# Performance work log

Hardware: AMD Instinct MI355X
Metric: run time of the kernel (lower is better)

Reference implementation:

```python
import jax, jax.numpy as jnp
import numpy as np

N_NODES = 50000
N_EDGES = 800000
D = 64
EPS = 1e-12  # torch F.normalize eps


def edge_softmax(e, dst, n):
    # softmax over incoming edges of each dst node, per feature channel
    m = jax.ops.segment_max(e, dst, num_segments=n)          # [N, D]
    ex = jnp.exp(e - m[dst])                                 # [E, D]
    s = jax.ops.segment_sum(ex, dst, num_segments=n)         # [N, D]
    return ex / s[dst]


def gat_layer(h, src, dst, W_src, b_src, W_dst, b_dst, n):
    # attention logits: u_mul_v
    e = h[src] * h[dst]                                      # [E, D]
    alpha = edge_softmax(e, dst, n)                          # [E, D]
    # transformed features (fc_dst computed in source but unused downstream)
    feat_src = jax.nn.relu(h @ W_src.T + b_src)              # [N, D]
    _feat_dst = jax.nn.relu(h @ W_dst.T + b_dst)             # [N, D] (dead, kept for fidelity)
    # message: u_mul_e, then scatter-sum to dst
    msg = feat_src[src] * alpha                              # [E, D]
    return jax.ops.segment_sum(msg, dst, num_segments=n)     # [N, D]


def l2_normalize(x):
    nrm = jnp.sqrt(jnp.sum(x * x, axis=1, keepdims=True))
    return x / jnp.maximum(nrm, EPS)


def setup_inputs() -> dict:
    key = jax.random.key(0)
    ks = jax.random.split(key, 10)
    scale = 1.0 / np.sqrt(D)
    return {
        "node_ids": jax.random.randint(ks[0], (N_NODES,), 0, N_NODES),
        "src": jax.random.randint(ks[1], (N_EDGES,), 0, N_NODES),
        "dst": jax.random.randint(ks[2], (N_EDGES,), 0, N_NODES),
        "embed_table": jax.random.normal(ks[3], (N_NODES, D), jnp.float32) * 0.1,
        "W_src_0": jax.random.normal(ks[4], (D, D), jnp.float32) * scale,
        "b_src_0": jnp.zeros((D,), jnp.float32),
        "W_dst_0": jax.random.normal(ks[5], (D, D), jnp.float32) * scale,
        "b_dst_0": jnp.zeros((D,), jnp.float32),
        "W_src_1": jax.random.normal(ks[6], (D, D), jnp.float32) * scale,
        "b_src_1": jnp.zeros((D,), jnp.float32),
        "W_dst_1": jax.random.normal(ks[7], (D, D), jnp.float32) * scale,
        "b_dst_1": jnp.zeros((D,), jnp.float32),
    }


def reference(node_ids, src, dst, embed_table,
              W_src_0, b_src_0, W_dst_0, b_dst_0,
              W_src_1, b_src_1, W_dst_1, b_dst_1):
    n = node_ids.shape[0]
    h0 = embed_table[node_ids]                               # [N, D]
    h1 = gat_layer(h0, src, dst, W_src_0, b_src_0, W_dst_0, b_dst_0, n)
    h2 = gat_layer(h1, src, dst, W_src_1, b_src_1, W_dst_1, b_dst_1, n)
    # cache = [h0, norm(h1), norm(h2)]; h passed forward unnormalized
    return jnp.concatenate([h0, l2_normalize(h1), l2_normalize(h2)], axis=1)  # [N, 3D]
```

## Files before the change

kernel.cpp:

```cpp
#include <hip/hip_runtime.h>
#include <math.h>

#define NN 50000
#define NE 800000
#define DD 64
#define FC_BLOCKS 782
#define N4 12500
#define ZB 49

typedef __attribute__((ext_vector_type(8))) short short8v;
typedef __attribute__((ext_vector_type(4))) float floatx4;

__device__ __forceinline__ unsigned bf16r(float x) {
  unsigned u = __float_as_uint(x);
  return (u + 0x7fffu + ((u >> 16) & 1u)) >> 16;
}


__global__ void k_hist(const int4* __restrict__ dst4, int* __restrict__ deg,
                       int4* __restrict__ pos4) {
  int q = blockIdx.x * 256 + threadIdx.x;
  if (q >= NE / 4) return;
  int4 dn = dst4[q];
  int4 p;
  p.x = atomicAdd(&deg[dn.x], 1);
  p.y = atomicAdd(&deg[dn.y], 1);
  p.z = atomicAdd(&deg[dn.z], 1);
  p.w = atomicAdd(&deg[dn.w], 1);
  pos4[q] = p;
}

__global__ void k_scan1(const int* __restrict__ deg, int* __restrict__ rp,
                        int* __restrict__ bsum) {
  __shared__ int woff[16];
  int t = threadIdx.x;
  int i = blockIdx.x * 1024 + t;
  int v = (i < NN) ? deg[i] : 0;
  int lane = t & 63, w = t >> 6;
  int sc = v;
#pragma unroll
  for (int off = 1; off < 64; off <<= 1) {
    int x = __shfl_up(sc, off, 64);
    if (lane >= off) sc += x;
  }
  if (lane == 63) woff[w] = sc;
  __syncthreads();
  if (t < 16) {
    int ws = woff[t];
    int s2 = ws;
#pragma unroll
    for (int off = 1; off < 16; off <<= 1) {
      int x = __shfl_up(s2, off, 64);
      if (t >= off) s2 += x;
    }
    woff[t] = s2 - ws;
    if (t == 15) bsum[blockIdx.x] = s2;
  }
  __syncthreads();
  if (i < NN) rp[i] = sc - v + woff[w];
}

__global__ void k_scan3(int* __restrict__ rp, const int* __restrict__ bsum) {
  __shared__ int soff;
  if (threadIdx.x < 64) {
    int v = ((int)threadIdx.x < (int)blockIdx.x) ? bsum[threadIdx.x] : 0;
#pragma unroll
    for (int off = 32; off > 0; off >>= 1) v += __shfl_xor(v, off, 64);
    if (threadIdx.x == 0) soff = v;
  }
  __syncthreads();
  int i = blockIdx.x * 1024 + threadIdx.x;
  if (i < NN) rp[i] += soff;
  if (i == 0) rp[NN] = NE;
}

__global__ void k_scatter(const int4* __restrict__ src4, const int4* __restrict__ dst4,
                          const int* __restrict__ rp, const int4* __restrict__ pos4,
                          int* __restrict__ ssrc) {
  int q = blockIdx.x * 256 + threadIdx.x;
  if (q >= NE / 4) return;
  int4 s = src4[q], dn = dst4[q], p = pos4[q];
  ssrc[rp[dn.x] + p.x] = s.x;
  ssrc[rp[dn.y] + p.y] = s.y;
  ssrc[rp[dn.z] + p.z] = s.z;
  ssrc[rp[dn.w] + p.w] = s.w;
}

__global__ void __launch_bounds__(256) k_fc_mfma(const float* __restrict__ h,
                                                 const int* __restrict__ ids,
                                                 const float* __restrict__ W,
                                                 const float* __restrict__ b,
                                                 unsigned* __restrict__ hfb,
                                                 int4* __restrict__ zbuf, int n4) {
  if (blockIdx.x >= FC_BLOCKS) {
    int i = (blockIdx.x - FC_BLOCKS) * 256 + threadIdx.x;
    if (i < n4) zbuf[i] = make_int4(0, 0, 0, 0);
    return;
  }
  int lane = threadIdx.x & 63;
  int wid = threadIdx.x >> 6;
  int nbase = blockIdx.x * 64 + wid * 16;
  if (nbase >= NN) return;
  int r16 = lane & 15, kg = lane >> 4;

  int rowA = ids ? ids[nbase + r16] : (nbase + r16);
  const float* hrow = h + (size_t)rowA * DD;
  short8v afr[2];
#pragma unroll
  for (int kt = 0; kt < 2; ++kt) {
    int k0 = kt * 32 + kg * 8;
#pragma unroll
    for (int i = 0; i < 8; ++i) afr[kt][i] = (short)bf16r(hrow[k0 + i]);
  }
  int orow[4];
#pragma unroll
  for (int r = 0; r < 4; ++r) {
    int node = nbase + kg * 4 + r;
    orow[r] = ids ? ids[node] : node;
  }
  short8v bfr[4][2];
#pragma unroll
  for (int dt = 0; dt < 4; ++dt) {
    const float* wrow = W + (dt * 16 + r16) * 64;
#pragma unroll
    for (int kt = 0; kt < 2; ++kt) {
      int k0 = kt * 32 + kg * 8;
#pragma unroll
      for (int i = 0; i < 8; ++i) bfr[dt][kt][i] = (short)bf16r(wrow[k0 + i]);
    }
  }
#pragma unroll
  for (int dt = 0; dt < 4; ++dt) {
    floatx4 acc = {0.f, 0.f, 0.f, 0.f};
    acc = __builtin_amdgcn_mfma_f32_16x16x32_bf16(afr[0], bfr[dt][0], acc, 0, 0, 0);
    acc = __builtin_amdgcn_mfma_f32_16x16x32_bf16(afr[1], bfr[dt][1], acc, 0, 0, 0);
    int d = dt * 16 + r16;
    float bias = b[d];
#pragma unroll
    for (int r = 0; r < 4; ++r) {
      int node = nbase + kg * 4 + r;
      float feat = fmaxf(acc[r] + bias, 0.f);
      float hv = h[(size_t)orow[r] * DD + d];
      hfb[node * DD + d] = bf16r(hv) | (bf16r(feat) << 16);
    }
  }
}

template <bool FINAL>
__global__ void __launch_bounds__(256)
k_edge_t(const unsigned* __restrict__ hfb, const float* __restrict__ h,
         const int* __restrict__ ids, const int* __restrict__ rp,
         const int* __restrict__ ssrc, float* __restrict__ outp, int ostride,
         const float* __restrict__ emb, const int* __restrict__ fids,
         const float* __restrict__ h1) {
  int d = threadIdx.x & 63;
  int node = __builtin_amdgcn_readfirstlane(blockIdx.x * 4 + (threadIdx.x >> 6));
  int beg = __builtin_amdgcn_readfirstlane(rp[node]);
  int end = __builtin_amdgcn_readfirstlane(rp[node + 1]);
  int hrow = ids ? __builtin_amdgcn_readfirstlane(ids[node]) : node;
  float hd = h[(size_t)hrow * DD + d] * 1.44269504f;
  const unsigned* hfb_d = hfb + d;
  float s[8] = {0.f, 0.f, 0.f, 0.f, 0.f, 0.f, 0.f, 0.f};
  float a[8] = {0.f, 0.f, 0.f, 0.f, 0.f, 0.f, 0.f, 0.f};
  int lim = end - 1;
  for (int p = beg; p < end; p += 8) {
    unsigned v[8];
#pragma unroll
    for (int j = 0; j < 8; ++j) {
      int q = p + j;
      q = (q > lim) ? lim : q;
      int sq = __builtin_amdgcn_readfirstlane(ssrc[q]);
      v[j] = hfb_d[(size_t)sq * DD];
    }
#pragma unroll
    for (int j = 0; j < 8; ++j) {
      float hv = __uint_as_float(v[j] << 16);
      float fv = __uint_as_float(v[j] & 0xffff0000u);
      float ex = __builtin_amdgcn_exp2f(hv * hd);
      s[j] += ex;
      a[j] = fmaf(fv, ex, a[j]);
    }
  }
  float ss = ((s[0] + s[1]) + (s[2] + s[3])) + ((s[4] + s[5]) + (s[6] + s[7]));
  float aa = ((a[0] + a[1]) + (a[2] + a[3])) + ((a[4] + a[5]) + (a[6] + a[7]));
  int deg = end - beg;
  if (deg > 0) {
    int dups = (8 - (deg & 7)) & 7;
    if (dups) {
      unsigned vL = hfb_d[(size_t)__builtin_amdgcn_readfirstlane(ssrc[lim]) * DD];
      float hvL = __uint_as_float(vL << 16);
      float fvL = __uint_as_float(vL & 0xffff0000u);
      float exL = __builtin_amdgcn_exp2f(hvL * hd);
      float fd = (float)dups;
      ss = fmaf(-fd, exL, ss);
      aa = fmaf(-fd * fvL, exL, aa);
    }
  }
  float hval = (deg > 0) ? aa / ss : 0.f;
  if (!FINAL) {
    outp[(size_t)node * ostride + d] = hval;
  } else {
    float v1 = h1[(size_t)node * DD + d];
    float s1 = v1 * v1, s2 = hval * hval;
#pragma unroll
    for (int off = 32; off > 0; off >>= 1) {
      s1 += __shfl_xor(s1, off, 64);
      s2 += __shfl_xor(s2, off, 64);
    }
    outp[node * 192 + d] = emb[(size_t)fids[node] * DD + d];
    outp[node * 192 + 64 + d] = v1 / fmaxf(sqrtf(s1), 1e-12f);
    outp[node * 192 + 128 + d] = hval / fmaxf(sqrtf(s2), 1e-12f);
  }
}


extern "C" void kernel_launch(void* const* d_in, const int* in_sizes, int n_in,
                              void* d_out, int out_size, void* d_ws, size_t ws_size,
                              hipStream_t stream) {
  const int* node_ids = (const int*)d_in[0];
  const int* src = (const int*)d_in[1];
  const int* dst = (const int*)d_in[2];
  const float* emb = (const float*)d_in[3];
  const float* W0 = (const float*)d_in[4];
  const float* b0 = (const float*)d_in[5];
  const float* W1 = (const float*)d_in[8];
  const float* b1 = (const float*)d_in[9];
  float* out = (float*)d_out;

  size_t o = 0;
  auto alloc = [&](size_t nbytes) {
    char* p = (char*)d_ws + o;
    o += (nbytes + 255) & ~(size_t)255;
    return (void*)p;
  };
  float* h1 = (float*)alloc((size_t)NN * DD * 4);
  unsigned* hfb = (unsigned*)alloc((size_t)NN * DD * 4);
  int* deg = (int*)alloc((size_t)(NN + 12) * 4);
  int* rp = (int*)alloc((size_t)(NN + 1) * 4);
  int* bsum = (int*)alloc(64 * 4);
  int* ssrc = (int*)alloc((size_t)NE * 4);
  int* pos = (int*)alloc((size_t)NE * 4);
  (void)o; (void)ws_size; (void)in_sizes; (void)n_in; (void)out_size;

  k_fc_mfma<<<FC_BLOCKS + ZB, 256, 0, stream>>>(emb, node_ids, W0, b0, hfb,
                                                (int4*)deg, N4);
  k_hist<<<(NE / 4 + 255) / 256, 256, 0, stream>>>((const int4*)dst, deg, (int4*)pos);
  int NB = (NN + 1023) / 1024;
  k_scan1<<<NB, 1024, 0, stream>>>(deg, rp, bsum);
  k_scan3<<<NB, 1024, 0, stream>>>(rp, bsum);
  k_scatter<<<(NE / 4 + 255) / 256, 256, 0, stream>>>(
      (const int4*)src, (const int4*)dst, rp, (const int4*)pos, ssrc);

  k_edge_t<false><<<(NN + 3) / 4, 256, 0, stream>>>(
      hfb, emb, node_ids, rp, ssrc, h1, DD, nullptr, nullptr, nullptr);
  k_fc_mfma<<<FC_BLOCKS, 256, 0, stream>>>(h1, nullptr, W1, b1, hfb, nullptr, 0);
  k_edge_t<true><<<(NN + 3) / 4, 256, 0, stream>>>(
      hfb, h1, nullptr, rp, ssrc, out, 0, emb, node_ids, h1);
}
```

Measured before the change: 161.8 us.

## Merge scan kernels and process two edges per wave in edge aggregation

Replaces the two-pass prefix scan with a single kernel in which each block redundantly sums all preceding degrees, removing one launch and the block-sum buffer. The degree buffer is enlarged and zeroed past NN so that rp[NN] comes out of the scan directly. The edge kernel now has each half-wave handle a different edge, with every lane covering two channels through 8-byte loads. The loop therefore takes 16 edges per iteration and combines the two halves with a cross-half shuffle at the end. This is meant to double the edges in flight per wave and halve the loop trip count, at the cost of more padding waste for low-degree nodes and more complex duplicate correction.

```diff
diff --git a/kernel.cpp b/kernel.cpp
--- a/kernel.cpp
+++ b/kernel.cpp
@@ -5,7 +5,7 @@
 #define NE 800000
 #define DD 64
 #define FC_BLOCKS 782
-#define N4 12500
+#define N4 12503
 #define ZB 49
 
 typedef __attribute__((ext_vector_type(8))) short short8v;
@@ -30,13 +30,27 @@
   pos4[q] = p;
 }
 
-__global__ void k_scan1(const int* __restrict__ deg, int* __restrict__ rp,
-                        int* __restrict__ bsum) {
+__global__ void k_scan(const int* __restrict__ deg, int* __restrict__ rp) {
+  __shared__ int wred[16];
   __shared__ int woff[16];
+  __shared__ int sbase;
   int t = threadIdx.x;
-  int i = blockIdx.x * 1024 + t;
+  int lane = t & 63, w = t >> 6;
+  int blockStart = blockIdx.x << 10;
+  int acc = 0;
+  for (int i = t; i < blockStart; i += 1024) acc += deg[i];
+#pragma unroll
+  for (int off = 32; off > 0; off >>= 1) acc += __shfl_xor(acc, off, 64);
+  if (lane == 0) wred[w] = acc;
+  __syncthreads();
+  if (t == 0) {
+    int b = 0;
+#pragma unroll
+    for (int k = 0; k < 16; ++k) b += wred[k];
+    sbase = b;
+  }
+  int i = blockStart + t;
   int v = (i < NN) ? deg[i] : 0;
-  int lane = t & 63, w = t >> 6;
   int sc = v;
 #pragma unroll
   for (int off = 1; off < 64; off <<= 1) {
@@ -54,24 +68,9 @@
       if (t >= off) s2 += x;
     }
     woff[t] = s2 - ws;
-    if (t == 15) bsum[blockIdx.x] = s2;
   }
   __syncthreads();
-  if (i < NN) rp[i] = sc - v + woff[w];
-}
-
-__global__ void k_scan3(int* __restrict__ rp, const int* __restrict__ bsum) {
-  __shared__ int soff;
-  if (threadIdx.x < 64) {
-    int v = ((int)threadIdx.x < (int)blockIdx.x) ? bsum[threadIdx.x] : 0;
-#pragma unroll
-    for (int off = 32; off > 0; off >>= 1) v += __shfl_xor(v, off, 64);
-    if (threadIdx.x == 0) soff = v;
-  }
-  __syncthreads();
-  int i = blockIdx.x * 1024 + threadIdx.x;
-  if (i < NN) rp[i] += soff;
-  if (i == 0) rp[NN] = NE;
+  if (i <= NN) rp[i] = sc - v + woff[w] + sbase;
 }
 
 __global__ void k_scatter(const int4* __restrict__ src4, const int4* __restrict__ dst4,
@@ -153,63 +152,100 @@
          const int* __restrict__ ssrc, float* __restrict__ outp, int ostride,
          const float* __restrict__ emb, const int* __restrict__ fids,
          const float* __restrict__ h1) {
-  int d = threadIdx.x & 63;
+  int lane = threadIdx.x & 63;
+  int half = lane >> 5;
+  int c = lane & 31;
   int node = __builtin_amdgcn_readfirstlane(blockIdx.x * 4 + (threadIdx.x >> 6));
   int beg = __builtin_amdgcn_readfirstlane(rp[node]);
   int end = __builtin_amdgcn_readfirstlane(rp[node + 1]);
   int hrow = ids ? __builtin_amdgcn_readfirstlane(ids[node]) : node;
-  float hd = h[(size_t)hrow * DD + d] * 1.44269504f;
-  const unsigned* hfb_d = hfb + d;
-  float s[8] = {0.f, 0.f, 0.f, 0.f, 0.f, 0.f, 0.f, 0.f};
-  float a[8] = {0.f, 0.f, 0.f, 0.f, 0.f, 0.f, 0.f, 0.f};
+  float2 hdv = *(const float2*)(h + (size_t)hrow * DD + 2 * c);
+  float hd0 = hdv.x * 1.44269504f;
+  float hd1 = hdv.y * 1.44269504f;
   int lim = end - 1;
-  for (int p = beg; p < end; p += 8) {
-    unsigned v[8];
+  float sA[8] = {0.f, 0.f, 0.f, 0.f, 0.f, 0.f, 0.f, 0.f};
+  float aA[8] = {0.f, 0.f, 0.f, 0.f, 0.f, 0.f, 0.f, 0.f};
+  float sB[8] = {0.f, 0.f, 0.f, 0.f, 0.f, 0.f, 0.f, 0.f};
+  float aB[8] = {0.f, 0.f, 0.f, 0.f, 0.f, 0.f, 0.f, 0.f};
+  for (int p = beg; p < end; p += 16) {
+    uint2 v[8];
 #pragma unroll
     for (int j = 0; j < 8; ++j) {
-      int q = p + j;
-      q = (q > lim) ? lim : q;
-      int sq = __builtin_amdgcn_readfirstlane(ssrc[q]);
-      v[j] = hfb_d[(size_t)sq * DD];
+      int q0 = p + 2 * j;
+      q0 = (q0 > lim) ? lim : q0;
+      int q1 = p + 2 * j + 1;
+      q1 = (q1 > lim) ? lim : q1;
+      int s0 = __builtin_amdgcn_readfirstlane(ssrc[q0]);
+      int s1 = __builtin_amdgcn_readfirstlane(ssrc[q1]);
+      int sq = half ? s1 : s0;
+      v[j] = *(const uint2*)(hfb + (size_t)sq * DD + 2 * c);
     }
 #pragma unroll
     for (int j = 0; j < 8; ++j) {
-      float hv = __uint_as_float(v[j] << 16);
-      float fv = __uint_as_float(v[j] & 0xffff0000u);
-      float ex = __builtin_amdgcn_exp2f(hv * hd);
-      s[j] += ex;
-      a[j] = fmaf(fv, ex, a[j]);
-    }
-  }
-  float ss = ((s[0] + s[1]) + (s[2] + s[3])) + ((s[4] + s[5]) + (s[6] + s[7]));
-  float aa = ((a[0] + a[1]) + (a[2] + a[3])) + ((a[4] + a[5]) + (a[6] + a[7]));
+      float hv0 = __uint_as_float(v[j].x << 16);
+      float fv0 = __uint_as_float(v[j].x & 0xffff0000u);
+      float hv1 = __uint_as_float(v[j].y << 16);
+      float fv1 = __uint_as_float(v[j].y & 0xffff0000u);
+      float e0 = __builtin_amdgcn_exp2f(hv0 * hd0);
+      float e1 = __builtin_amdgcn_exp2f(hv1 * hd1);
+      sA[j] += e0;
+      aA[j] = fmaf(fv0, e0, aA[j]);
+      sB[j] += e1;
+      aB[j] = fmaf(fv1, e1, aB[j]);
+    }
+  }
+  float ss0 = ((sA[0] + sA[1]) + (sA[2] + sA[3])) + ((sA[4] + sA[5]) + (sA[6] + sA[7]));
+  float aa0 = ((aA[0] + aA[1]) + (aA[2] + aA[3])) + ((aA[4] + aA[5]) + (aA[6] + aA[7]));
+  float ss1 = ((sB[0] + sB[1]) + (sB[2] + sB[3])) + ((sB[4] + sB[5]) + (sB[6] + sB[7]));
+  float aa1 = ((aB[0] + aB[1]) + (aB[2] + aB[3])) + ((aB[4] + aB[5]) + (aB[6] + aB[7]));
   int deg = end - beg;
   if (deg > 0) {
-    int dups = (8 - (deg & 7)) & 7;
-    if (dups) {
-      unsigned vL = hfb_d[(size_t)__builtin_amdgcn_readfirstlane(ssrc[lim]) * DD];
-      float hvL = __uint_as_float(vL << 16);
-      float fvL = __uint_as_float(vL & 0xffff0000u);
-      float exL = __builtin_amdgcn_exp2f(hvL * hd);
-      float fd = (float)dups;
-      ss = fmaf(-fd, exL, ss);
-      aa = fmaf(-fd * fvL, exL, aa);
-    }
-  }
-  float hval = (deg > 0) ? aa / ss : 0.f;
+    int rem = deg & 15;
+    if (rem) {
+      int dups0 = (rem & 1) ? (16 - rem) >> 1 : (17 - rem) >> 1;
+      int dups1 = (16 - rem) - dups0;
+      float fd = (float)(half ? dups1 : dups0);
+      int sL = __builtin_amdgcn_readfirstlane(ssrc[lim]);
+      uint2 vL = *(const uint2*)(hfb + (size_t)sL * DD + 2 * c);
+      float hvL0 = __uint_as_float(vL.x << 16);
+      float fvL0 = __uint_as_float(vL.x & 0xffff0000u);
+      float hvL1 = __uint_as_float(vL.y << 16);
+      float fvL1 = __uint_as_float(vL.y & 0xffff0000u);
+      float eL0 = __builtin_amdgcn_exp2f(hvL0 * hd0);
+      float eL1 = __builtin_amdgcn_exp2f(hvL1 * hd1);
+      ss0 = fmaf(-fd, eL0, ss0);
+      aa0 = fmaf(-fd * fvL0, eL0, aa0);
+      ss1 = fmaf(-fd, eL1, ss1);
+      aa1 = fmaf(-fd * fvL1, eL1, aa1);
+    }
+    ss0 += __shfl_xor(ss0, 32, 64);
+    aa0 += __shfl_xor(aa0, 32, 64);
+    ss1 += __shfl_xor(ss1, 32, 64);
+    aa1 += __shfl_xor(aa1, 32, 64);
+  }
+  float hv0 = (deg > 0) ? aa0 / ss0 : 0.f;
+  float hv1 = (deg > 0) ? aa1 / ss1 : 0.f;
   if (!FINAL) {
-    outp[(size_t)node * ostride + d] = hval;
+    if (half == 0)
+      *(float2*)(outp + (size_t)node * ostride + 2 * c) = make_float2(hv0, hv1);
   } else {
-    float v1 = h1[(size_t)node * DD + d];
-    float s1 = v1 * v1, s2 = hval * hval;
-#pragma unroll
-    for (int off = 32; off > 0; off >>= 1) {
-      s1 += __shfl_xor(s1, off, 64);
-      s2 += __shfl_xor(s2, off, 64);
-    }
-    outp[node * 192 + d] = emb[(size_t)fids[node] * DD + d];
-    outp[node * 192 + 64 + d] = v1 / fmaxf(sqrtf(s1), 1e-12f);
-    outp[node * 192 + 128 + d] = hval / fmaxf(sqrtf(s2), 1e-12f);
+    float2 v1 = *(const float2*)(h1 + (size_t)node * DD + 2 * c);
+    float ps1 = v1.x * v1.x + v1.y * v1.y;
+    float ps2 = hv0 * hv0 + hv1 * hv1;
+#pragma unroll
+    for (int off = 16; off > 0; off >>= 1) {
+      ps1 += __shfl_xor(ps1, off, 64);
+      ps2 += __shfl_xor(ps2, off, 64);
+    }
+    float inv1 = 1.f / fmaxf(sqrtf(ps1), 1e-12f);
+    float inv2 = 1.f / fmaxf(sqrtf(ps2), 1e-12f);
+    if (half == 0) {
+      int fr = __builtin_amdgcn_readfirstlane(fids[node]);
+      float2 e2 = *(const float2*)(emb + (size_t)fr * DD + 2 * c);
+      *(float2*)(outp + node * 192 + 2 * c) = e2;
+      *(float2*)(outp + node * 192 + 64 + 2 * c) = make_float2(v1.x * inv1, v1.y * inv1);
+      *(float2*)(outp + node * 192 + 128 + 2 * c) = make_float2(hv0 * inv2, hv1 * inv2);
+    }
   }
 }
 
@@ -235,9 +271,8 @@
   };
   float* h1 = (float*)alloc((size_t)NN * DD * 4);
   unsigned* hfb = (unsigned*)alloc((size_t)NN * DD * 4);
-  int* deg = (int*)alloc((size_t)(NN + 12) * 4);
+  int* deg = (int*)alloc((size_t)N4 * 16);
   int* rp = (int*)alloc((size_t)(NN + 1) * 4);
-  int* bsum = (int*)alloc(64 * 4);
   int* ssrc = (int*)alloc((size_t)NE * 4);
   int* pos = (int*)alloc((size_t)NE * 4);
   (void)o; (void)ws_size; (void)in_sizes; (void)n_in; (void)out_size;
@@ -246,8 +281,7 @@
                                                 (int4*)deg, N4);
   k_hist<<<(NE / 4 + 255) / 256, 256, 0, stream>>>((const int4*)dst, deg, (int4*)pos);
   int NB = (NN + 1023) / 1024;
-  k_scan1<<<NB, 1024, 0, stream>>>(deg, rp, bsum);
-  k_scan3<<<NB, 1024, 0, stream>>>(rp, bsum);
+  k_scan<<<NB, 1024, 0, stream>>>(deg, rp);
   k_scatter<<<(NE / 4 + 255) / 256, 256, 0, stream>>>(
       (const int4*)src, (const int4*)dst, rp, (const int4*)pos, ssrc);
 
```

Result: slower. 169.3 us (+4.7%).

## Fuse scan into single kernel and software-pipeline edge gather loads

Applied to the files above, without the earlier changes.

Merges the two-pass exclusive scan into one kernel in which each block first reduces all preceding degrees itself, removing a launch and the block-sum buffer. rp[NN] is now written by the scan, so the deg buffer is padded and the zeroing count raised to keep index NN zero. The edge aggregation loop is double-buffered: the next eight gathered rows are loaded while the current ones go through exp and accumulate. The padding correction reuses the last computed exp instead of reloading it. Later scan blocks repeat redundant prefix reads, and the doubled load registers may lower occupancy.

```diff
diff --git a/kernel.cpp b/kernel.cpp
--- a/kernel.cpp
+++ b/kernel.cpp
@@ -5,7 +5,7 @@
 #define NE 800000
 #define DD 64
 #define FC_BLOCKS 782
-#define N4 12500
+#define N4 12503
 #define ZB 49
 
 typedef __attribute__((ext_vector_type(8))) short short8v;
@@ -30,13 +30,27 @@
   pos4[q] = p;
 }
 
-__global__ void k_scan1(const int* __restrict__ deg, int* __restrict__ rp,
-                        int* __restrict__ bsum) {
+__global__ void k_scan(const int* __restrict__ deg, int* __restrict__ rp) {
+  __shared__ int wred[16];
   __shared__ int woff[16];
+  __shared__ int sbase;
   int t = threadIdx.x;
-  int i = blockIdx.x * 1024 + t;
+  int lane = t & 63, w = t >> 6;
+  int blockStart = blockIdx.x << 10;
+  int acc = 0;
+  for (int i = t; i < blockStart; i += 1024) acc += deg[i];
+#pragma unroll
+  for (int off = 32; off > 0; off >>= 1) acc += __shfl_xor(acc, off, 64);
+  if (lane == 0) wred[w] = acc;
+  __syncthreads();
+  if (t == 0) {
+    int b = 0;
+#pragma unroll
+    for (int k = 0; k < 16; ++k) b += wred[k];
+    sbase = b;
+  }
+  int i = blockStart + t;
   int v = (i < NN) ? deg[i] : 0;
-  int lane = t & 63, w = t >> 6;
   int sc = v;
 #pragma unroll
   for (int off = 1; off < 64; off <<= 1) {
@@ -54,24 +68,9 @@
       if (t >= off) s2 += x;
     }
     woff[t] = s2 - ws;
-    if (t == 15) bsum[blockIdx.x] = s2;
   }
   __syncthreads();
-  if (i < NN) rp[i] = sc - v + woff[w];
-}
-
-__global__ void k_scan3(int* __restrict__ rp, const int* __restrict__ bsum) {
-  __shared__ int soff;
-  if (threadIdx.x < 64) {
-    int v = ((int)threadIdx.x < (int)blockIdx.x) ? bsum[threadIdx.x] : 0;
-#pragma unroll
-    for (int off = 32; off > 0; off >>= 1) v += __shfl_xor(v, off, 64);
-    if (threadIdx.x == 0) soff = v;
-  }
-  __syncthreads();
-  int i = blockIdx.x * 1024 + threadIdx.x;
-  if (i < NN) rp[i] += soff;
-  if (i == 0) rp[NN] = NE;
+  if (i <= NN) rp[i] = sc - v + woff[w] + sbase;
 }
 
 __global__ void k_scatter(const int4* __restrict__ src4, const int4* __restrict__ dst4,
@@ -160,18 +159,39 @@
   int hrow = ids ? __builtin_amdgcn_readfirstlane(ids[node]) : node;
   float hd = h[(size_t)hrow * DD + d] * 1.44269504f;
   const unsigned* hfb_d = hfb + d;
-  float s[8] = {0.f, 0.f, 0.f, 0.f, 0.f, 0.f, 0.f, 0.f};
-  float a[8] = {0.f, 0.f, 0.f, 0.f, 0.f, 0.f, 0.f, 0.f};
+  int deg = end - beg;
   int lim = end - 1;
-  for (int p = beg; p < end; p += 8) {
+  float ss = 0.f, aa = 0.f;
+  if (deg > 0) {
+    float s[8] = {0.f, 0.f, 0.f, 0.f, 0.f, 0.f, 0.f, 0.f};
+    float a[8] = {0.f, 0.f, 0.f, 0.f, 0.f, 0.f, 0.f, 0.f};
     unsigned v[8];
 #pragma unroll
     for (int j = 0; j < 8; ++j) {
-      int q = p + j;
+      int q = beg + j;
       q = (q > lim) ? lim : q;
-      int sq = __builtin_amdgcn_readfirstlane(ssrc[q]);
-      v[j] = hfb_d[(size_t)sq * DD];
-    }
+      v[j] = hfb_d[(size_t)__builtin_amdgcn_readfirstlane(ssrc[q]) * DD];
+    }
+    for (int p = beg + 8; p < end; p += 8) {
+      unsigned w[8];
+#pragma unroll
+      for (int j = 0; j < 8; ++j) {
+        int q = p + j;
+        q = (q > lim) ? lim : q;
+        w[j] = hfb_d[(size_t)__builtin_amdgcn_readfirstlane(ssrc[q]) * DD];
+      }
+#pragma unroll
+      for (int j = 0; j < 8; ++j) {
+        float hv = __uint_as_float(v[j] << 16);
+        float fv = __uint_as_float(v[j] & 0xffff0000u);
+        float ex = __builtin_amdgcn_exp2f(hv * hd);
+        s[j] += ex;
+        a[j] = fmaf(fv, ex, a[j]);
+      }
+#pragma unroll
+      for (int j = 0; j < 8; ++j) v[j] = w[j];
+    }
+    float e7 = 0.f, f7 = 0.f;
 #pragma unroll
     for (int j = 0; j < 8; ++j) {
       float hv = __uint_as_float(v[j] << 16);
@@ -179,21 +199,15 @@
       float ex = __builtin_amdgcn_exp2f(hv * hd);
       s[j] += ex;
       a[j] = fmaf(fv, ex, a[j]);
-    }
-  }
-  float ss = ((s[0] + s[1]) + (s[2] + s[3])) + ((s[4] + s[5]) + (s[6] + s[7]));
-  float aa = ((a[0] + a[1]) + (a[2] + a[3])) + ((a[4] + a[5]) + (a[6] + a[7]));
-  int deg = end - beg;
-  if (deg > 0) {
+      if (j == 7) { e7 = ex; f7 = fv; }
+    }
+    ss = ((s[0] + s[1]) + (s[2] + s[3])) + ((s[4] + s[5]) + (s[6] + s[7]));
+    aa = ((a[0] + a[1]) + (a[2] + a[3])) + ((a[4] + a[5]) + (a[6] + a[7]));
     int dups = (8 - (deg & 7)) & 7;
     if (dups) {
-      unsigned vL = hfb_d[(size_t)__builtin_amdgcn_readfirstlane(ssrc[lim]) * DD];
-      float hvL = __uint_as_float(vL << 16);
-      float fvL = __uint_as_float(vL & 0xffff0000u);
-      float exL = __builtin_amdgcn_exp2f(hvL * hd);
       float fd = (float)dups;
-      ss = fmaf(-fd, exL, ss);
-      aa = fmaf(-fd * fvL, exL, aa);
+      ss = fmaf(-fd, e7, ss);
+      aa = fmaf(-fd * f7, e7, aa);
     }
   }
   float hval = (deg > 0) ? aa / ss : 0.f;
@@ -235,9 +249,8 @@
   };
   float* h1 = (float*)alloc((size_t)NN * DD * 4);
   unsigned* hfb = (unsigned*)alloc((size_t)NN * DD * 4);
-  int* deg = (int*)alloc((size_t)(NN + 12) * 4);
+  int* deg = (int*)alloc((size_t)N4 * 16);
   int* rp = (int*)alloc((size_t)(NN + 1) * 4);
-  int* bsum = (int*)alloc(64 * 4);
   int* ssrc = (int*)alloc((size_t)NE * 4);
   int* pos = (int*)alloc((size_t)NE * 4);
   (void)o; (void)ws_size; (void)in_sizes; (void)n_in; (void)out_size;
@@ -246,8 +259,7 @@
                                                 (int4*)deg, N4);
   k_hist<<<(NE / 4 + 255) / 256, 256, 0, stream>>>((const int4*)dst, deg, (int4*)pos);
   int NB = (NN + 1023) / 1024;
-  k_scan1<<<NB, 1024, 0, stream>>>(deg, rp, bsum);
-  k_scan3<<<NB, 1024, 0, stream>>>(rp, bsum);
+  k_scan<<<NB, 1024, 0, stream>>>(deg, rp);
   k_scatter<<<(NE / 4 + 255) / 256, 256, 0, stream>>>(
       (const int4*)src, (const int4*)dst, rp, (const int4*)pos, ssrc);
 
```

Result: no change. 164.8 us (+1.9%).
